# Kernel optimization log

Measured on AMD Instinct MI355X. Metric: run time of the kernel, lower is better.

The kernel has to match this reference:

```python
import jax, jax.numpy as jnp
import numpy as np

B, NX, NY, D_FEAT, CTX, S, T = 64, 32, 32, 1024, 512, 32, 4
N = NX * NY


def build_adjacency_matrix(nx, ny):
    # 4-neighborhood grid adjacency with self loops (faithful to original loop)
    adj = np.eye(nx * ny, dtype=np.float32)
    row = 0
    for i in range(nx):
        for j in range(ny):
            if i > 0:
                adj[row, j + (i - 1) * nx] = 1.0
            if i < nx - 1:
                adj[row, j + (i + 1) * nx] = 1.0
            if j > 0:
                adj[row, j - 1 + i * nx] = 1.0
            if j < ny - 1:
                adj[row, j + 1 + i * nx] = 1.0
            row += 1
    return adj


def setup_inputs() -> dict:
    key = jax.random.key(0)
    ks = jax.random.split(key, 12)
    s = 0.02
    return {
        "images": jax.random.normal(ks[0], (B, N, D_FEAT), jnp.float32),
        "q_encoding": jax.random.normal(ks[1], (B, CTX), jnp.float32),
        "lstm_outputs": jax.random.normal(ks[2], (B, S, CTX), jnp.float32),
        "q_length": jax.random.randint(ks[3], (B,), 1, S + 1, jnp.int32),
        "adj": jnp.asarray(build_adjacency_matrix(NX, NY)),
        "initKB_w": jax.random.normal(ks[4], (CTX, D_FEAT), jnp.float32) * s,
        "initKB_b": jnp.zeros((CTX,), jnp.float32),
        "W_w": jax.random.normal(ks[5], (CTX, 2 * CTX), jnp.float32) * s,
        "W_b": jnp.zeros((CTX,), jnp.float32),
        "qInput_w": jax.random.normal(ks[6], (CTX, CTX), jnp.float32) * s,
        "qInput_b": jnp.zeros((CTX,), jnp.float32),
        "qInputT_w": jax.random.normal(ks[7], (T, CTX, CTX), jnp.float32) * s,
        "qInputT_b": jnp.zeros((T, CTX), jnp.float32),
        "cmd_w": jax.random.normal(ks[8], (1, CTX), jnp.float32) * s,
        "cmd_b": jnp.zeros((1,), jnp.float32),
    }


def reference(images, q_encoding, lstm_outputs, q_length, adj,
              initKB_w, initKB_b, W_w, W_b, qInput_w, qInput_b,
              qInputT_w, qInputT_b, cmd_w, cmd_b) -> jnp.ndarray:
    n_iter = qInputT_w.shape[0]
    seq = lstm_outputs.shape[1]
    # loc_init: images [B,N,D_FEAT] -> x_loc [B,N,CTX]
    x_loc = jnp.einsum("bnd,cd->bnc", images, initKB_w) + initKB_b
    # shared first command layer (cfg.CMD_INPUT_ACT = elu)
    q1 = jax.nn.elu(q_encoding @ qInput_w.T + qInput_b)  # [B,CTX]
    valid = jnp.arange(seq)[None, :] < q_length[:, None]  # [B,S]
    for t in range(n_iter):
        # extract_textual_command
        q_cmd = q1 @ qInputT_w[t].T + qInputT_b[t]  # [B,CTX]
        raw_att = jnp.einsum("bsd,d->bs", q_cmd[:, None, :] * lstm_outputs, cmd_w[0]) + cmd_b[0]
        raw_att = jnp.where(valid, raw_att, -1e30)
        att = jax.nn.softmax(raw_att, axis=-1)  # [B,S]
        cmd = jnp.einsum("bs,bsd->bd", att, lstm_outputs)  # [B,CTX]
        # propagate_message: concat + linear, then dense adjacency matmul
        cmd_tiled = jnp.broadcast_to(cmd[:, None, :], x_loc.shape)
        support = jnp.concatenate([x_loc, cmd_tiled], axis=-1) @ W_w.T + W_b  # [B,N,CTX]
        x_new = jnp.einsum("nm,bmd->bnd", adj, support)  # [B,N,CTX]
        x_loc = jax.nn.elu(x_new) if t < n_iter - 1 else x_new
    return x_loc
```

## Files before the change

kernel.cpp:

```cpp
#include <hip/hip_runtime.h>
#include <hip/hip_bf16.h>
#include <math.h>

#define NB 64
#define NNODES 1024
#define CTXD 512
#define SEQL 32

typedef __attribute__((ext_vector_type(8))) short short8;
typedef __attribute__((ext_vector_type(4))) float floatx4;

__device__ __forceinline__ float bf2f(unsigned short u) {
  union { unsigned int i; float f; } v; v.i = ((unsigned int)u) << 16; return v.f;
}
__device__ __forceinline__ unsigned short f2bf(float f) {
  union { float f; unsigned int i; } v; v.f = f;
  unsigned int r = v.i + 0x7fffu + ((v.i >> 16) & 1u);
  return (unsigned short)(r >> 16);
}
__device__ __forceinline__ float elu1(float x) { return x > 0.f ? x : expm1f(x); }

__device__ __forceinline__ void gload16(const void* g, void* l) {
  __builtin_amdgcn_global_load_lds((const __attribute__((address_space(1))) void*)g,
                                   (__attribute__((address_space(3))) void*)l, 16, 0, 0);
}

__global__ __launch_bounds__(256) void pack_k(const float* __restrict__ kbw,
                                              const float* __restrict__ Ww,
                                              const float* __restrict__ qiw,
                                              const float* __restrict__ qtw,
                                              unsigned short* __restrict__ kb_bf,
                                              unsigned short* __restrict__ w1_bf,
                                              float* __restrict__ qiT,
                                              float* __restrict__ qTT,
                                              float* __restrict__ w2T) {
  int idx = blockIdx.x * 256 + threadIdx.x;
  if (idx < 524288) {
    kb_bf[idx] = f2bf(kbw[idx]);
  } else if (idx < 786432) {
    int o = idx - 524288;
    w1_bf[o] = f2bf(Ww[(o >> 9) * 1024 + (o & 511)]);
  } else if (idx < 1048576) {
    int o = idx - 786432;
    int k = o >> 9, c = o & 511;
    qiT[o] = qiw[c * 512 + k];
  } else if (idx < 2097152) {
    int o = idx - 1048576;
    int t = o >> 18, r = o & 262143;
    int k = r >> 9, c = r & 511;
    qTT[o] = qtw[((size_t)t * 512 + c) * 512 + k];
  } else {
    int o = idx - 2097152;
    int k = o >> 9, c = o & 511;
    w2T[o] = Ww[c * 1024 + 512 + k];
  }
}

__global__ __launch_bounds__(512) void q1_k(const float* __restrict__ q_enc,
                                            const float* __restrict__ qiT,
                                            const float* __restrict__ qInput_b,
                                            float* __restrict__ q1) {
  int b = blockIdx.x, c = threadIdx.x;
  __shared__ float qes[512];
  qes[c] = q_enc[b * 512 + c];
  __syncthreads();
  float a0 = qInput_b[c], a1 = 0.f, a2 = 0.f, a3 = 0.f;
#pragma unroll 4
  for (int k = 0; k < 512; k += 4) {
    a0 += qes[k] * qiT[k * 512 + c];
    a1 += qes[k + 1] * qiT[(k + 1) * 512 + c];
    a2 += qes[k + 2] * qiT[(k + 2) * 512 + c];
    a3 += qes[k + 3] * qiT[(k + 3) * 512 + c];
  }
  q1[b * 512 + c] = elu1(a0 + a1 + a2 + a3);
}

__global__ __launch_bounds__(512) void cmdt_k(
    const float* __restrict__ q1, const float* __restrict__ lstm,
    const int* __restrict__ q_len,
    const float* __restrict__ qTT, const float* __restrict__ qT_b,
    const float* __restrict__ cmd_w, const float* __restrict__ cmd_b,
    const float* __restrict__ w2T, const float* __restrict__ W_b,
    float* __restrict__ bias2) {
  int b = blockIdx.x & 63;
  int t = blockIdx.x >> 6;
  int c = threadIdx.x;
  __shared__ float q1s[512];
  __shared__ float us[512];
  __shared__ float red[512];
  __shared__ float atts[32];
  __shared__ float cmds[512];

  q1s[c] = q1[b * 512 + c];
  __syncthreads();

  const float* wt = qTT + (size_t)t * 262144;
  float a0 = qT_b[t * 512 + c], a1 = 0.f, a2 = 0.f, a3 = 0.f;
#pragma unroll 4
  for (int k = 0; k < 512; k += 4) {
    a0 += q1s[k] * wt[k * 512 + c];
    a1 += q1s[k + 1] * wt[(k + 1) * 512 + c];
    a2 += q1s[k + 2] * wt[(k + 2) * 512 + c];
    a3 += q1s[k + 3] * wt[(k + 3) * 512 + c];
  }
  us[c] = (a0 + a1 + a2 + a3) * cmd_w[c];
  __syncthreads();

  const float* lstmb = lstm + (size_t)b * SEQL * 512;
  {
    int s = c >> 4, u = c & 15;
    float p = 0.f;
    const float* lr = lstmb + s * 512;
    for (int r = u; r < 512; r += 16) p += us[r] * lr[r];
    red[c] = p;
  }
  __syncthreads();
  if (c < 32) {
    float raw = cmd_b[0];
    for (int u = 0; u < 16; u++) raw += red[c * 16 + u];
    raw = (c < q_len[b]) ? raw : -1e30f;
    float mx = raw;
    for (int off = 16; off; off >>= 1) mx = fmaxf(mx, __shfl_xor(mx, off, 32));
    float e = expf(raw - mx);
    float sm = e;
    for (int off = 16; off; off >>= 1) sm += __shfl_xor(sm, off, 32);
    atts[c] = e / sm;
  }
  __syncthreads();
  float cd = 0.f;
#pragma unroll
  for (int s = 0; s < 32; s++) cd += atts[s] * lstmb[s * 512 + c];
  cmds[c] = cd;
  __syncthreads();

  float b0 = W_b[c], b1 = 0.f, b2 = 0.f, b3 = 0.f;
#pragma unroll 4
  for (int k = 0; k < 512; k += 4) {
    b0 += cmds[k] * w2T[k * 512 + c];
    b1 += cmds[k + 1] * w2T[(k + 1) * 512 + c];
    b2 += cmds[k + 2] * w2T[(k + 2) * 512 + c];
    b3 += cmds[k + 3] * w2T[(k + 3) * 512 + c];
  }
  bias2[((size_t)(t * 64 + b)) * 512 + c] = b0 + b1 + b2 + b3;
}

template <int AMODE, int MODE>
__global__ __launch_bounds__(256, 3) void tgemm(
    const void* __restrict__ Ap, int lda,
    const unsigned short* __restrict__ Bw, int ldb, int K,
    const float* __restrict__ cbias, const float* __restrict__ bias2,
    void* __restrict__ Cp) {
  __shared__ __align__(128) unsigned short As[64 * 64];
  __shared__ __align__(128) unsigned short Bs[256 * 64];

  const int tid = threadIdx.x;
  const int lane = tid & 63;
  const int wn = tid >> 6;
  const int lr = lane & 15;
  const int lk = lane >> 4;
  const int lr7 = lr & 7;

  int bid = blockIdx.x;
  int cpx = gridDim.x >> 3;
  int wg = (bid & 7) * cpx + (bid >> 3);
  const size_t rowBase = (size_t)(wg >> 1) * 64;
  const int colBase = (wg & 1) * 256;

  floatx4 acc[4][4];
#pragma unroll
  for (int m = 0; m < 4; m++)
#pragma unroll
    for (int n = 0; n < 4; n++) acc[m][n] = {0.f, 0.f, 0.f, 0.f};

  for (int k0 = 0; k0 < K; k0 += 64) {
    __syncthreads();
    if constexpr (AMODE == 0) {
      const float* Af = (const float*)Ap;
#pragma unroll
      for (int j = 0; j < 2; j++) {
        int g = j * 256 + tid;
        int r = g >> 3, u = g & 7;
        const float* src = Af + (rowBase + r) * (size_t)lda + k0 + u * 8;
        floatx4 v0 = *(const floatx4*)src;
        floatx4 v1 = *(const floatx4*)(src + 4);
        short8 t;
#pragma unroll
        for (int e = 0; e < 4; e++) {
          t[e] = (short)f2bf(v0[e]);
          t[e + 4] = (short)f2bf(v1[e]);
        }
        *(short8*)((char*)As + r * 128 + ((u ^ (r & 7)) << 4)) = t;
      }
    } else {
      const unsigned short* X = (const unsigned short*)Ap;
#pragma unroll
      for (int j = 0; j < 2; j++) {
        int g = j * 256 + tid;
        int r = g >> 3, u = g & 7;
        size_t R = rowBase + r;
        int n = (int)(R & 1023);
        int gi = n >> 5, gj = n & 31;
        const unsigned short* p = X + R * 512 + k0 + u * 8;
        short8 c = *(const short8*)p;
        float s[8];
#pragma unroll
        for (int e = 0; e < 8; e++) s[e] = bf2f((unsigned short)c[e]);
        if (gi > 0) {
          short8 t = *(const short8*)(p - 32 * 512);
#pragma unroll
          for (int e = 0; e < 8; e++) s[e] += bf2f((unsigned short)t[e]);
        }
        if (gi < 31) {
          short8 t = *(const short8*)(p + 32 * 512);
#pragma unroll
          for (int e = 0; e < 8; e++) s[e] += bf2f((unsigned short)t[e]);
        }
        if (gj > 0) {
          short8 t = *(const short8*)(p - 512);
#pragma unroll
          for (int e = 0; e < 8; e++) s[e] += bf2f((unsigned short)t[e]);
        }
        if (gj < 31) {
          short8 t = *(const short8*)(p + 512);
#pragma unroll
          for (int e = 0; e < 8; e++) s[e] += bf2f((unsigned short)t[e]);
        }
        short8 o;
#pragma unroll
        for (int e = 0; e < 8; e++) o[e] = (short)f2bf(s[e]);
        *(short8*)((char*)As + r * 128 + ((u ^ (r & 7)) << 4)) = o;
      }
    }
#pragma unroll
    for (int j = 0; j < 8; j++) {
      int g = j * 256 + tid;
      int r = g >> 3, u = g & 7;
      gload16(Bw + (size_t)(colBase + r) * ldb + k0 + ((u ^ (r & 7)) << 3),
              (char*)Bs + g * 16);
    }
    __syncthreads();

#pragma unroll
    for (int kk = 0; kk < 2; kk++) {
      const int ub = ((kk << 2) + lk) ^ lr7;
      short8 a[4], b[4];
#pragma unroll
      for (int m = 0; m < 4; m++)
        a[m] = *(const short8*)((const char*)As + (m * 16 + lr) * 128 + (ub << 4));
#pragma unroll
      for (int n = 0; n < 4; n++)
        b[n] = *(const short8*)((const char*)Bs + (wn * 64 + n * 16 + lr) * 128 + (ub << 4));
#pragma unroll
      for (int m = 0; m < 4; m++)
#pragma unroll
        for (int n = 0; n < 4; n++)
          acc[m][n] = __builtin_amdgcn_mfma_f32_16x16x32_bf16(a[m], b[n], acc[m][n], 0, 0, 0);
    }
  }

#pragma unroll
  for (int m = 0; m < 4; m++) {
#pragma unroll
    for (int q = 0; q < 4; q++) {
      size_t grow = rowBase + m * 16 + lk * 4 + q;
      float degf = 0.f;
      const float* b2 = nullptr;
      if constexpr (MODE != 0) {
        int nsp = (int)(grow & 1023);
        int ii = nsp >> 5, jj = nsp & 31;
        degf = (float)(1 + (ii > 0) + (ii < 31) + (jj > 0) + (jj < 31));
        b2 = bias2 + (grow >> 10) * CTXD;
      }
#pragma unroll
      for (int n = 0; n < 4; n++) {
        int gcol = colBase + wn * 64 + n * 16 + lr;
        float v = acc[m][n][q];
        if constexpr (MODE == 0) v += cbias[gcol];
        else v += degf * b2[gcol];
        if constexpr (MODE == 1) v = elu1(v);
        if constexpr (MODE == 2) ((float*)Cp)[grow * CTXD + gcol] = v;
        else ((unsigned short*)Cp)[grow * CTXD + gcol] = f2bf(v);
      }
    }
  }
}

extern "C" void kernel_launch(void* const* d_in, const int* in_sizes, int n_in,
                              void* d_out, int out_size, void* d_ws, size_t ws_size,
                              hipStream_t stream) {
  const float* images   = (const float*)d_in[0];
  const float* q_enc    = (const float*)d_in[1];
  const float* lstm     = (const float*)d_in[2];
  const int*   q_len    = (const int*)d_in[3];
  const float* initKB_w = (const float*)d_in[5];
  const float* initKB_b = (const float*)d_in[6];
  const float* W_w      = (const float*)d_in[7];
  const float* W_b      = (const float*)d_in[8];
  const float* qInput_w = (const float*)d_in[9];
  const float* qInput_b = (const float*)d_in[10];
  const float* qT_w     = (const float*)d_in[11];
  const float* qT_b     = (const float*)d_in[12];
  const float* cmd_w    = (const float*)d_in[13];
  const float* cmd_b    = (const float*)d_in[14];

  char* ws = (char*)d_ws;
  unsigned short* X1    = (unsigned short*)ws;
  float*          qiT   = (float*)ws;
  float*          qTT   = (float*)(ws + 1048576);
  float*          w2T   = (float*)(ws + 5242880);
  unsigned short* kb_bf = (unsigned short*)(ws + 67108864);
  unsigned short* w1_bf = (unsigned short*)(ws + 68157440);
  float*          bias2 = (float*)(ws + 68681728);
  float*          q1    = (float*)(ws + 69206016);
  unsigned short* X0    = (unsigned short*)d_out;

  pack_k<<<9216, 256, 0, stream>>>(initKB_w, W_w, qInput_w, qT_w,
                                   kb_bf, w1_bf, qiT, qTT, w2T);
  q1_k<<<64, 512, 0, stream>>>(q_enc, qiT, qInput_b, q1);
  cmdt_k<<<256, 512, 0, stream>>>(q1, lstm, q_len, qTT, qT_b, cmd_w, cmd_b,
                                  w2T, W_b, bias2);

  tgemm<0, 0><<<2048, 256, 0, stream>>>(images, 1024, kb_bf, 1024, 1024,
                                        initKB_b, nullptr, X0);

  tgemm<1, 1><<<2048, 256, 0, stream>>>(X0, 512, w1_bf, 512, 512,
                                        nullptr, bias2 + 0 * 32768, X1);
  tgemm<1, 1><<<2048, 256, 0, stream>>>(X1, 512, w1_bf, 512, 512,
                                        nullptr, bias2 + 1 * 32768, X0);
  tgemm<1, 1><<<2048, 256, 0, stream>>>(X0, 512, w1_bf, 512, 512,
                                        nullptr, bias2 + 2 * 32768, X1);
  tgemm<1, 2><<<2048, 256, 0, stream>>>(X1, 512, w1_bf, 512, 512,
                                        nullptr, bias2 + 3 * 32768, d_out);
}
```

Baseline: 531.7 us.

## Load weight fragments directly from global and widen tiles to full output width

The GEMM kernel no longer stages the weight tile in LDS. Each wave now reads its B fragments straight from global memory (relying on cache), and each block covers all 512 output columns instead of 256, so the grid is halved. This removes the LDS staging and its bandwidth, and the A tile is gathered once per row block instead of twice. The cost is uncoalesced-ish global loads of B inside the MFMA loop with no prefetch, plus a doubled accumulator array that raises register pressure (launch bounds lowered to 2 blocks).

```diff
diff --git a/kernel.cpp b/kernel.cpp
--- a/kernel.cpp
+++ b/kernel.cpp
@@ -19,11 +19,6 @@
   return (unsigned short)(r >> 16);
 }
 __device__ __forceinline__ float elu1(float x) { return x > 0.f ? x : expm1f(x); }
-
-__device__ __forceinline__ void gload16(const void* g, void* l) {
-  __builtin_amdgcn_global_load_lds((const __attribute__((address_space(1))) void*)g,
-                                   (__attribute__((address_space(3))) void*)l, 16, 0, 0);
-}
 
 __global__ __launch_bounds__(256) void pack_k(const float* __restrict__ kbw,
                                               const float* __restrict__ Ww,
@@ -144,14 +139,13 @@
   bias2[((size_t)(t * 64 + b)) * 512 + c] = b0 + b1 + b2 + b3;
 }
 
-template <int AMODE, int MODE>
-__global__ __launch_bounds__(256, 3) void tgemm(
-    const void* __restrict__ Ap, int lda,
-    const unsigned short* __restrict__ Bw, int ldb, int K,
+template <int AMODE, int MODE, int K>
+__global__ __launch_bounds__(256, 2) void dgemm(
+    const void* __restrict__ Ap,
+    const unsigned short* __restrict__ Bw,
     const float* __restrict__ cbias, const float* __restrict__ bias2,
     void* __restrict__ Cp) {
   __shared__ __align__(128) unsigned short As[64 * 64];
-  __shared__ __align__(128) unsigned short Bs[256 * 64];
 
   const int tid = threadIdx.x;
   const int lane = tid & 63;
@@ -161,16 +155,14 @@
   const int lr7 = lr & 7;
 
   int bid = blockIdx.x;
-  int cpx = gridDim.x >> 3;
-  int wg = (bid & 7) * cpx + (bid >> 3);
-  const size_t rowBase = (size_t)(wg >> 1) * 64;
-  const int colBase = (wg & 1) * 256;
-
-  floatx4 acc[4][4];
+  int wg = (bid & 7) * (gridDim.x >> 3) + (bid >> 3);
+  const size_t rowBase = (size_t)wg * 64;
+
+  floatx4 acc[4][8];
 #pragma unroll
   for (int m = 0; m < 4; m++)
 #pragma unroll
-    for (int n = 0; n < 4; n++) acc[m][n] = {0.f, 0.f, 0.f, 0.f};
+    for (int n = 0; n < 8; n++) acc[m][n] = {0.f, 0.f, 0.f, 0.f};
 
   for (int k0 = 0; k0 < K; k0 += 64) {
     __syncthreads();
@@ -180,7 +172,7 @@
       for (int j = 0; j < 2; j++) {
         int g = j * 256 + tid;
         int r = g >> 3, u = g & 7;
-        const float* src = Af + (rowBase + r) * (size_t)lda + k0 + u * 8;
+        const float* src = Af + (rowBase + r) * (size_t)K + k0 + u * 8;
         floatx4 v0 = *(const floatx4*)src;
         floatx4 v1 = *(const floatx4*)(src + 4);
         short8 t;
@@ -200,7 +192,7 @@
         size_t R = rowBase + r;
         int n = (int)(R & 1023);
         int gi = n >> 5, gj = n & 31;
-        const unsigned short* p = X + R * 512 + k0 + u * 8;
+        const unsigned short* p = X + R * (size_t)K + k0 + u * 8;
         short8 c = *(const short8*)p;
         float s[8];
 #pragma unroll
@@ -231,29 +223,23 @@
         *(short8*)((char*)As + r * 128 + ((u ^ (r & 7)) << 4)) = o;
       }
     }
-#pragma unroll
-    for (int j = 0; j < 8; j++) {
-      int g = j * 256 + tid;
-      int r = g >> 3, u = g & 7;
-      gload16(Bw + (size_t)(colBase + r) * ldb + k0 + ((u ^ (r & 7)) << 3),
-              (char*)Bs + g * 16);
-    }
     __syncthreads();
 
 #pragma unroll
     for (int kk = 0; kk < 2; kk++) {
       const int ub = ((kk << 2) + lk) ^ lr7;
-      short8 a[4], b[4];
+      short8 a[4], b[8];
+#pragma unroll
+      for (int n = 0; n < 8; n++)
+        b[n] = *(const short8*)(Bw + (size_t)(wn * 128 + n * 16 + lr) * K +
+                                k0 + (kk << 5) + (lk << 3));
 #pragma unroll
       for (int m = 0; m < 4; m++)
-        a[m] = *(const short8*)((const char*)As + (m * 16 + lr) * 128 + (ub << 4));
-#pragma unroll
-      for (int n = 0; n < 4; n++)
-        b[n] = *(const short8*)((const char*)Bs + (wn * 64 + n * 16 + lr) * 128 + (ub << 4));
+        a[m] = *(const short8*)((const char*)As + ((m * 16 + lr) << 7) + (ub << 4));
 #pragma unroll
       for (int m = 0; m < 4; m++)
 #pragma unroll
-        for (int n = 0; n < 4; n++)
+        for (int n = 0; n < 8; n++)
           acc[m][n] = __builtin_amdgcn_mfma_f32_16x16x32_bf16(a[m], b[n], acc[m][n], 0, 0, 0);
     }
   }
@@ -272,8 +258,8 @@
         b2 = bias2 + (grow >> 10) * CTXD;
       }
 #pragma unroll
-      for (int n = 0; n < 4; n++) {
-        int gcol = colBase + wn * 64 + n * 16 + lr;
+      for (int n = 0; n < 8; n++) {
+        int gcol = wn * 128 + n * 16 + lr;
         float v = acc[m][n][q];
         if constexpr (MODE == 0) v += cbias[gcol];
         else v += degf * b2[gcol];
@@ -320,15 +306,15 @@
   cmdt_k<<<256, 512, 0, stream>>>(q1, lstm, q_len, qTT, qT_b, cmd_w, cmd_b,
                                   w2T, W_b, bias2);
 
-  tgemm<0, 0><<<2048, 256, 0, stream>>>(images, 1024, kb_bf, 1024, 1024,
-                                        initKB_b, nullptr, X0);
-
-  tgemm<1, 1><<<2048, 256, 0, stream>>>(X0, 512, w1_bf, 512, 512,
-                                        nullptr, bias2 + 0 * 32768, X1);
-  tgemm<1, 1><<<2048, 256, 0, stream>>>(X1, 512, w1_bf, 512, 512,
-                                        nullptr, bias2 + 1 * 32768, X0);
-  tgemm<1, 1><<<2048, 256, 0, stream>>>(X0, 512, w1_bf, 512, 512,
-                                        nullptr, bias2 + 2 * 32768, X1);
-  tgemm<1, 2><<<2048, 256, 0, stream>>>(X1, 512, w1_bf, 512, 512,
-                                        nullptr, bias2 + 3 * 32768, d_out);
-}
+  dgemm<0, 0, 1024><<<1024, 256, 0, stream>>>(images, kb_bf,
+                                              initKB_b, nullptr, X0);
+
+  dgemm<1, 1, 512><<<1024, 256, 0, stream>>>(X0, w1_bf,
+                                             nullptr, bias2 + 0 * 32768, X1);
+  dgemm<1, 1, 512><<<1024, 256, 0, stream>>>(X1, w1_bf,
+                                             nullptr, bias2 + 1 * 32768, X0);
+  dgemm<1, 1, 512><<<1024, 256, 0, stream>>>(X0, w1_bf,
+                                             nullptr, bias2 + 2 * 32768, X1);
+  dgemm<1, 2, 512><<<1024, 256, 0, stream>>>(X1, w1_bf,
+                                             nullptr, bias2 + 3 * 32768, d_out);
+}
```

After: 791.5 us. +48.9%, slower.

## Pipeline stencil-fused message GEMM with double-buffered LDS and 128-row tiles

Applied to the files above, without the earlier changes.

Splits the generic templated GEMM into a plain input-projection GEMM and a new fused stencil GEMM for the four propagation steps. The new kernel uses 512 threads with 128x256 tiles and double-buffered LDS. Stencil neighbour loads are issued two k-steps ahead, using branchless clamped addresses and float masks, and are interleaved with async B loads under explicit vmcnt waits and sched barriers. This is meant to hide global load latency behind MFMA work and raise reuse of the B operand. In exchange it adds register and LDS pressure and relies on fragile hand-counted waitcnt values.

```diff
diff --git a/kernel.cpp b/kernel.cpp
--- a/kernel.cpp
+++ b/kernel.cpp
@@ -144,12 +144,11 @@
   bias2[((size_t)(t * 64 + b)) * 512 + c] = b0 + b1 + b2 + b3;
 }
 
-template <int AMODE, int MODE>
-__global__ __launch_bounds__(256, 3) void tgemm(
-    const void* __restrict__ Ap, int lda,
-    const unsigned short* __restrict__ Bw, int ldb, int K,
-    const float* __restrict__ cbias, const float* __restrict__ bias2,
-    void* __restrict__ Cp) {
+__global__ __launch_bounds__(256, 3) void igemm(
+    const float* __restrict__ Af,
+    const unsigned short* __restrict__ Bw,
+    const float* __restrict__ cbias,
+    unsigned short* __restrict__ Cp) {
   __shared__ __align__(128) unsigned short As[64 * 64];
   __shared__ __align__(128) unsigned short Bs[256 * 64];
 
@@ -161,8 +160,7 @@
   const int lr7 = lr & 7;
 
   int bid = blockIdx.x;
-  int cpx = gridDim.x >> 3;
-  int wg = (bid & 7) * cpx + (bid >> 3);
+  int wg = (bid & 7) * (gridDim.x >> 3) + (bid >> 3);
   const size_t rowBase = (size_t)(wg >> 1) * 64;
   const int colBase = (wg & 1) * 256;
 
@@ -172,70 +170,28 @@
 #pragma unroll
     for (int n = 0; n < 4; n++) acc[m][n] = {0.f, 0.f, 0.f, 0.f};
 
-  for (int k0 = 0; k0 < K; k0 += 64) {
+  for (int k0 = 0; k0 < 1024; k0 += 64) {
     __syncthreads();
-    if constexpr (AMODE == 0) {
-      const float* Af = (const float*)Ap;
-#pragma unroll
-      for (int j = 0; j < 2; j++) {
-        int g = j * 256 + tid;
-        int r = g >> 3, u = g & 7;
-        const float* src = Af + (rowBase + r) * (size_t)lda + k0 + u * 8;
-        floatx4 v0 = *(const floatx4*)src;
-        floatx4 v1 = *(const floatx4*)(src + 4);
-        short8 t;
-#pragma unroll
-        for (int e = 0; e < 4; e++) {
-          t[e] = (short)f2bf(v0[e]);
-          t[e + 4] = (short)f2bf(v1[e]);
-        }
-        *(short8*)((char*)As + r * 128 + ((u ^ (r & 7)) << 4)) = t;
+#pragma unroll
+    for (int j = 0; j < 2; j++) {
+      int g = j * 256 + tid;
+      int r = g >> 3, u = g & 7;
+      const float* src = Af + (rowBase + r) * (size_t)1024 + k0 + u * 8;
+      floatx4 v0 = *(const floatx4*)src;
+      floatx4 v1 = *(const floatx4*)(src + 4);
+      short8 t;
+#pragma unroll
+      for (int e = 0; e < 4; e++) {
+        t[e] = (short)f2bf(v0[e]);
+        t[e + 4] = (short)f2bf(v1[e]);
       }
-    } else {
-      const unsigned short* X = (const unsigned short*)Ap;
-#pragma unroll
-      for (int j = 0; j < 2; j++) {
-        int g = j * 256 + tid;
-        int r = g >> 3, u = g & 7;
-        size_t R = rowBase + r;
-        int n = (int)(R & 1023);
-        int gi = n >> 5, gj = n & 31;
-        const unsigned short* p = X + R * 512 + k0 + u * 8;
-        short8 c = *(const short8*)p;
-        float s[8];
-#pragma unroll
-        for (int e = 0; e < 8; e++) s[e] = bf2f((unsigned short)c[e]);
-        if (gi > 0) {
-          short8 t = *(const short8*)(p - 32 * 512);
-#pragma unroll
-          for (int e = 0; e < 8; e++) s[e] += bf2f((unsigned short)t[e]);
-        }
-        if (gi < 31) {
-          short8 t = *(const short8*)(p + 32 * 512);
-#pragma unroll
-          for (int e = 0; e < 8; e++) s[e] += bf2f((unsigned short)t[e]);
-        }
-        if (gj > 0) {
-          short8 t = *(const short8*)(p - 512);
-#pragma unroll
-          for (int e = 0; e < 8; e++) s[e] += bf2f((unsigned short)t[e]);
-        }
-        if (gj < 31) {
-          short8 t = *(const short8*)(p + 512);
-#pragma unroll
-          for (int e = 0; e < 8; e++) s[e] += bf2f((unsigned short)t[e]);
-        }
-        short8 o;
-#pragma unroll
-        for (int e = 0; e < 8; e++) o[e] = (short)f2bf(s[e]);
-        *(short8*)((char*)As + r * 128 + ((u ^ (r & 7)) << 4)) = o;
-      }
+      *(short8*)((char*)As + r * 128 + ((u ^ (r & 7)) << 4)) = t;
     }
 #pragma unroll
     for (int j = 0; j < 8; j++) {
       int g = j * 256 + tid;
       int r = g >> 3, u = g & 7;
-      gload16(Bw + (size_t)(colBase + r) * ldb + k0 + ((u ^ (r & 7)) << 3),
+      gload16(Bw + (size_t)(colBase + r) * 1024 + k0 + ((u ^ (r & 7)) << 3),
               (char*)Bs + g * 16);
     }
     __syncthreads();
@@ -263,23 +219,181 @@
 #pragma unroll
     for (int q = 0; q < 4; q++) {
       size_t grow = rowBase + m * 16 + lk * 4 + q;
-      float degf = 0.f;
-      const float* b2 = nullptr;
-      if constexpr (MODE != 0) {
-        int nsp = (int)(grow & 1023);
-        int ii = nsp >> 5, jj = nsp & 31;
-        degf = (float)(1 + (ii > 0) + (ii < 31) + (jj > 0) + (jj < 31));
-        b2 = bias2 + (grow >> 10) * CTXD;
-      }
 #pragma unroll
       for (int n = 0; n < 4; n++) {
         int gcol = colBase + wn * 64 + n * 16 + lr;
-        float v = acc[m][n][q];
-        if constexpr (MODE == 0) v += cbias[gcol];
-        else v += degf * b2[gcol];
-        if constexpr (MODE == 1) v = elu1(v);
-        if constexpr (MODE == 2) ((float*)Cp)[grow * CTXD + gcol] = v;
-        else ((unsigned short*)Cp)[grow * CTXD + gcol] = f2bf(v);
+        Cp[grow * CTXD + gcol] = f2bf(acc[m][n][q] + cbias[gcol]);
+      }
+    }
+  }
+}
+
+struct Taps { short8 c, up, dn, lf, rt; };
+
+template <int MODE>
+__global__ __launch_bounds__(512, 2) void fgemm(
+    const unsigned short* __restrict__ X,
+    const unsigned short* __restrict__ Bw,
+    const float* __restrict__ bias2,
+    void* __restrict__ Cp) {
+  __shared__ __align__(128) unsigned short AsL[2][128 * 64];
+  __shared__ __align__(128) unsigned short BsL[2][256 * 64];
+
+  const int tid = threadIdx.x;
+  const int lane = tid & 63;
+  const int wave = tid >> 6;
+  const int wm = wave >> 2;
+  const int wn = wave & 3;
+  const int lr = lane & 15;
+  const int lk = lane >> 4;
+  const int lr7 = lr & 7;
+
+  int bid = blockIdx.x;
+  int wg = (bid & 7) * (gridDim.x >> 3) + (bid >> 3);
+  const size_t rowBase = (size_t)(wg >> 1) * 128;
+  const int colBase = (wg & 1) * 256;
+
+  floatx4 acc[4][4];
+#pragma unroll
+  for (int m = 0; m < 4; m++)
+#pragma unroll
+    for (int n = 0; n < 4; n++) acc[m][n] = {0.f, 0.f, 0.f, 0.f};
+
+  const int rl = tid >> 3;
+  const int uu = tid & 7;
+
+  auto issueT = [&](Taps& T, int h, int kt) {
+    size_t R = rowBase + h * 64 + rl;
+    int n = (int)(R & 1023);
+    const unsigned short* p = X + R * 512 + kt * 64 + uu * 8;
+    T.c = *(const short8*)p;
+    T.up = *(const short8*)(p + (((n >> 5) > 0) ? -32 * 512 : 0));
+    T.dn = *(const short8*)(p + (((n >> 5) < 31) ? 32 * 512 : 0));
+    T.lf = *(const short8*)(p + (((n & 31) > 0) ? -512 : 0));
+    T.rt = *(const short8*)(p + (((n & 31) < 31) ? 512 : 0));
+  };
+  auto commitT = [&](const Taps& T, int h, int d) {
+    int r = h * 64 + rl;
+    size_t R = rowBase + r;
+    int n = (int)(R & 1023);
+    float mu = ((n >> 5) > 0) ? 1.f : 0.f;
+    float md = ((n >> 5) < 31) ? 1.f : 0.f;
+    float ml = ((n & 31) > 0) ? 1.f : 0.f;
+    float mr = ((n & 31) < 31) ? 1.f : 0.f;
+    short8 o;
+#pragma unroll
+    for (int e = 0; e < 8; e++) {
+      float s = bf2f((unsigned short)T.c[e]);
+      s += mu * bf2f((unsigned short)T.up[e]);
+      s += md * bf2f((unsigned short)T.dn[e]);
+      s += ml * bf2f((unsigned short)T.lf[e]);
+      s += mr * bf2f((unsigned short)T.rt[e]);
+      o[e] = (short)f2bf(s);
+    }
+    *(short8*)((char*)&AsL[d][0] + r * 128 + ((uu ^ (r & 7)) << 4)) = o;
+  };
+  auto stgB = [&](int d, int h, int kt) {
+#pragma unroll
+    for (int j = 0; j < 2; j++) {
+      int g = h * 1024 + j * 512 + tid;
+      int r = g >> 3, u = g & 7;
+      gload16(Bw + (size_t)(colBase + r) * 512 + kt * 64 + ((u ^ (r & 7)) << 3),
+              (char*)&BsL[d][0] + g * 16);
+    }
+  };
+  auto phase = [&](int d, int kk) {
+    const char* Ab = (const char*)&AsL[d][0];
+    const char* Bb = (const char*)&BsL[d][0];
+    const int ub = ((kk << 2) + lk) ^ lr7;
+    short8 a[4], b[4];
+#pragma unroll
+    for (int m = 0; m < 4; m++)
+      a[m] = *(const short8*)(Ab + (wm * 64 + m * 16 + lr) * 128 + (ub << 4));
+#pragma unroll
+    for (int n = 0; n < 4; n++)
+      b[n] = *(const short8*)(Bb + (wn * 64 + n * 16 + lr) * 128 + (ub << 4));
+    asm volatile("s_waitcnt lgkmcnt(0)" ::: "memory");
+    __builtin_amdgcn_sched_barrier(0);
+    __builtin_amdgcn_s_setprio(1);
+#pragma unroll
+    for (int m = 0; m < 4; m++)
+#pragma unroll
+      for (int n = 0; n < 4; n++)
+        acc[m][n] = __builtin_amdgcn_mfma_f32_16x16x32_bf16(a[m], b[n], acc[m][n], 0, 0, 0);
+    __builtin_amdgcn_s_setprio(0);
+    __builtin_amdgcn_sched_barrier(0);
+  };
+
+  Taps tH0, tH1;
+
+  issueT(tH0, 0, 0);
+  issueT(tH1, 1, 0);
+  __builtin_amdgcn_sched_barrier(0);
+  stgB(0, 0, 0);
+  stgB(0, 1, 0);
+  __builtin_amdgcn_sched_barrier(0);
+  asm volatile("s_waitcnt vmcnt(9)" ::: "memory");
+  __builtin_amdgcn_sched_barrier(0);
+  commitT(tH0, 0, 0);
+  asm volatile("s_waitcnt vmcnt(4)" ::: "memory");
+  __builtin_amdgcn_sched_barrier(0);
+  commitT(tH1, 1, 0);
+  issueT(tH0, 0, 1);
+  issueT(tH1, 1, 1);
+  __builtin_amdgcn_sched_barrier(0);
+  asm volatile("s_waitcnt vmcnt(10)" ::: "memory");
+  asm volatile("s_waitcnt lgkmcnt(0)" ::: "memory");
+  __builtin_amdgcn_sched_barrier(0);
+  __builtin_amdgcn_s_barrier();
+  __builtin_amdgcn_sched_barrier(0);
+
+  for (int t = 0; t < 8; t++) {
+    const int cur = t & 1, nxt = cur ^ 1;
+    const int ktn = (t + 1) & 7, kt2 = (t + 2) & 7;
+
+    stgB(nxt, 0, ktn);
+    __builtin_amdgcn_sched_barrier(0);
+    phase(cur, 0);
+    asm volatile("s_waitcnt vmcnt(7)" ::: "memory");
+    __builtin_amdgcn_sched_barrier(0);
+    commitT(tH0, 0, nxt);
+    __builtin_amdgcn_sched_barrier(0);
+
+    stgB(nxt, 1, ktn);
+    __builtin_amdgcn_sched_barrier(0);
+    phase(cur, 1);
+    asm volatile("s_waitcnt vmcnt(4)" ::: "memory");
+    __builtin_amdgcn_sched_barrier(0);
+    commitT(tH1, 1, nxt);
+    issueT(tH0, 0, kt2);
+    issueT(tH1, 1, kt2);
+    __builtin_amdgcn_sched_barrier(0);
+    asm volatile("s_waitcnt vmcnt(10)" ::: "memory");
+    asm volatile("s_waitcnt lgkmcnt(0)" ::: "memory");
+    __builtin_amdgcn_sched_barrier(0);
+    __builtin_amdgcn_s_barrier();
+    __builtin_amdgcn_sched_barrier(0);
+  }
+  asm volatile("s_waitcnt vmcnt(0)" ::: "memory");
+
+#pragma unroll
+  for (int m = 0; m < 4; m++) {
+#pragma unroll
+    for (int q = 0; q < 4; q++) {
+      size_t grow = rowBase + wm * 64 + m * 16 + lk * 4 + q;
+      int nsp = (int)(grow & 1023);
+      int ii = nsp >> 5, jj = nsp & 31;
+      float degf = (float)(1 + (ii > 0) + (ii < 31) + (jj > 0) + (jj < 31));
+      const float* b2 = bias2 + (grow >> 10) * CTXD;
+#pragma unroll
+      for (int n = 0; n < 4; n++) {
+        int gcol = colBase + wn * 64 + n * 16 + lr;
+        float v = acc[m][n][q] + degf * b2[gcol];
+        if constexpr (MODE == 1) {
+          ((unsigned short*)Cp)[grow * CTXD + gcol] = f2bf(elu1(v));
+        } else {
+          ((float*)Cp)[grow * CTXD + gcol] = v;
+        }
       }
     }
   }
@@ -320,15 +434,10 @@
   cmdt_k<<<256, 512, 0, stream>>>(q1, lstm, q_len, qTT, qT_b, cmd_w, cmd_b,
                                   w2T, W_b, bias2);
 
-  tgemm<0, 0><<<2048, 256, 0, stream>>>(images, 1024, kb_bf, 1024, 1024,
-                                        initKB_b, nullptr, X0);
-
-  tgemm<1, 1><<<2048, 256, 0, stream>>>(X0, 512, w1_bf, 512, 512,
-                                        nullptr, bias2 + 0 * 32768, X1);
-  tgemm<1, 1><<<2048, 256, 0, stream>>>(X1, 512, w1_bf, 512, 512,
-                                        nullptr, bias2 + 1 * 32768, X0);
-  tgemm<1, 1><<<2048, 256, 0, stream>>>(X0, 512, w1_bf, 512, 512,
-                                        nullptr, bias2 + 2 * 32768, X1);
-  tgemm<1, 2><<<2048, 256, 0, stream>>>(X1, 512, w1_bf, 512, 512,
-                                        nullptr, bias2 + 3 * 32768, d_out);
-}
+  igemm<<<2048, 256, 0, stream>>>(images, kb_bf, initKB_b, X0);
+
+  fgemm<1><<<1024, 512, 0, stream>>>(X0, w1_bf, bias2 + 0 * 32768, X1);
+  fgemm<1><<<1024, 512, 0, stream>>>(X1, w1_bf, bias2 + 1 * 32768, X0);
+  fgemm<1><<<1024, 512, 0, stream>>>(X0, w1_bf, bias2 + 2 * 32768, X1);
+  fgemm<2><<<1024, 512, 0, stream>>>(X1, w1_bf, bias2 + 3 * 32768, d_out);
+}
```

After: 567.6 us. +6.7%, slower.
